# Kernel optimization log

Hardware: AMD Instinct MI355X
Metric: run time of the kernel (lower is better)

## Reference

```python
import jax, jax.numpy as jnp
import numpy as np

PAD_ID, BOS_ID, EOS_ID = 0, 2, 3
NHEAD = 8


def _sincos(T, d):
    pos = jnp.arange(T, dtype=jnp.float32)
    omega = jnp.exp(-jnp.arange(0, d, 2, dtype=jnp.float32) * (np.log(10000.0) / d))
    out = pos[:, None] * omega[None, :]  # [T, d/2]
    return jnp.stack([jnp.sin(out), jnp.cos(out)], axis=2).reshape(T, d)[None]  # [1,T,d]


def _ln(x, g, b, eps=1e-5):
    mu = x.mean(-1, keepdims=True)
    var = ((x - mu) ** 2).mean(-1, keepdims=True)
    return (x - mu) / jnp.sqrt(var + eps) * g + b


def _mha(q_in, kv_in, wqkv, bqkv, wo, bo, mask):
    B, Tq, d = q_in.shape
    Tk = kv_in.shape[1]
    hd = d // NHEAD
    q = q_in @ wqkv[:d].T + bqkv[:d]
    k = kv_in @ wqkv[d:2 * d].T + bqkv[d:2 * d]
    v = kv_in @ wqkv[2 * d:].T + bqkv[2 * d:]
    q = q.reshape(B, Tq, NHEAD, hd).transpose(0, 2, 1, 3)
    k = k.reshape(B, Tk, NHEAD, hd).transpose(0, 2, 1, 3)
    v = v.reshape(B, Tk, NHEAD, hd).transpose(0, 2, 1, 3)
    s = jnp.einsum('bhqd,bhkd->bhqk', q, k) / np.sqrt(hd)
    if mask is not None:
        s = s + mask
    a = jax.nn.softmax(s, axis=-1)
    o = jnp.einsum('bhqk,bhkd->bhqd', a, v).transpose(0, 2, 1, 3).reshape(B, Tq, d)
    return o @ wo.T + bo


def _last_logits(tokens, state, emb_table, qkv_w, qkv_b, out_w, out_b,
                 ffn_w1, ffn_b1, ffn_w2, ffn_b2, ln_g, ln_b):
    T = tokens.shape[1]
    d = emb_table.shape[1]
    x = emb_table[tokens] * np.sqrt(d) + _sincos(T, d)
    mask = jnp.where(jnp.tril(jnp.ones((T, T), bool)), 0.0, -jnp.inf)
    L = qkv_w.shape[0]
    for l in range(L):
        x = _ln(x + _mha(x, x, qkv_w[l, 0], qkv_b[l, 0], out_w[l, 0], out_b[l, 0], mask), ln_g[l, 0], ln_b[l, 0])
        x = _ln(x + _mha(x, state, qkv_w[l, 1], qkv_b[l, 1], out_w[l, 1], out_b[l, 1], None), ln_g[l, 1], ln_b[l, 1])
        h = jax.nn.gelu(x @ ffn_w1[l].T + ffn_b1[l], approximate=False)
        x = _ln(x + h @ ffn_w2[l].T + ffn_b2[l], ln_g[l, 2], ln_b[l, 2])
    return x[:, -1, :] @ emb_table.T  # tied output projection


def setup_inputs() -> dict:
    key = jax.random.key(0)
    ks = jax.random.split(key, 8)
    V, d, L, dff, B, K = 32000, 512, 4, 2048, 8, 64
    s = 0.02
    emb = jax.random.normal(ks[1], (V, d), jnp.float32) * s
    emb = emb.at[PAD_ID].set(0.0)  # padding_idx row is zero
    return {
        'state': jax.random.normal(ks[0], (B, K, d), jnp.float32),
        'emb_table': emb,
        'qkv_w': jax.random.normal(ks[2], (L, 2, 3 * d, d), jnp.float32) * s,
        'qkv_b': jnp.zeros((L, 2, 3 * d), jnp.float32),
        'out_w': jax.random.normal(ks[3], (L, 2, d, d), jnp.float32) * s,
        'out_b': jnp.zeros((L, 2, d), jnp.float32),
        'ffn_w1': jax.random.normal(ks[4], (L, dff, d), jnp.float32) * s,
        'ffn_b1': jnp.zeros((L, dff), jnp.float32),
        'ffn_w2': jax.random.normal(ks[5], (L, d, dff), jnp.float32) * s,
        'ffn_b2': jnp.zeros((L, d), jnp.float32),
        'ln_g': jnp.ones((L, 3, d), jnp.float32),
        'ln_b': jnp.zeros((L, 3, d), jnp.float32),
        'max_length': 16,
        'top_k': 50,
    }


def reference(state, emb_table, qkv_w, qkv_b, out_w, out_b, ffn_w1, ffn_b1,
              ffn_w2, ffn_b2, ln_g, ln_b, max_length, top_k):
    B = state.shape[0]
    generated = jnp.full((B, 1), BOS_ID, dtype=jnp.int32)
    finished = jnp.zeros(B, dtype=bool)
    key = jax.random.key(1)
    temperature = 1.0
    for t in range(max_length):
        # faithful naive recompute: full self+cross attention over generated prefix
        logits = _last_logits(generated, state, emb_table, qkv_w, qkv_b, out_w, out_b,
                              ffn_w1, ffn_b1, ffn_w2, ffn_b2, ln_g, ln_b)
        logits = logits / max(temperature, 1e-8)
        thr = jax.lax.top_k(logits, top_k)[0][:, -1:]
        filt = jnp.where(logits < thr, -jnp.inf, logits)
        nxt = jax.random.categorical(jax.random.fold_in(key, t), filt, axis=-1)
        nxt = jnp.where(finished, PAD_ID, nxt).astype(jnp.int32)
        generated = jnp.concatenate([generated, nxt[:, None]], axis=1)
        finished = finished | (nxt == EOS_ID)
    return generated
```

## Files before the change

kernel.cpp:

```cpp
#include <hip/hip_runtime.h>
#include <math.h>
#include <stdint.h>

#define D     512
#define DFF   2048
#define BB    8
#define NH    8
#define HD    64
#define NV    32000
#define NL    4
#define TMAX  17
#define KC    64
#define STEPS 16
#define KTOP  50
#define PAD_ID 0
#define BOS_ID 2
#define EOS_ID 3
#define SCOPE __HIP_MEMORY_SCOPE_AGENT

__device__ __forceinline__ float ld1(const float* p) {
  return __hip_atomic_load(p, __ATOMIC_RELAXED, SCOPE);
}
__device__ __forceinline__ void st1(float* p, float v) {
  __hip_atomic_store(p, v, __ATOMIC_RELAXED, SCOPE);
}
__device__ __forceinline__ float2 ld2(const float* p) {
  union { double d; float2 f; } u;
  u.d = __hip_atomic_load((const double*)p, __ATOMIC_RELAXED, SCOPE);
  return u.f;
}
__device__ __forceinline__ unsigned ldu(const unsigned* p) {
  return __hip_atomic_load(p, __ATOMIC_RELAXED, SCOPE);
}

__device__ __forceinline__ void tf2x32(unsigned k0, unsigned k1, unsigned x0, unsigned x1,
                                       unsigned& o0, unsigned& o1)
{
  unsigned ks2 = k0 ^ k1 ^ 0x1BD11BDAu;
#define TFR(r) { x0 += x1; x1 = (x1 << (r)) | (x1 >> (32 - (r))); x1 ^= x0; }
  x0 += k0; x1 += k1;
  TFR(13) TFR(15) TFR(26) TFR(6)
  x0 += k1;  x1 += ks2 + 1u;
  TFR(17) TFR(29) TFR(16) TFR(24)
  x0 += ks2; x1 += k0 + 2u;
  TFR(13) TFR(15) TFR(26) TFR(6)
  x0 += k0;  x1 += k1 + 3u;
  TFR(17) TFR(29) TFR(16) TFR(24)
  x0 += k1;  x1 += ks2 + 4u;
  TFR(13) TFR(15) TFR(26) TFR(6)
  o0 = x0 + ks2; o1 = x1 + k0 + 5u;
#undef TFR
}

__device__ __forceinline__ float wredf(float v) {
  for (int o = 32; o; o >>= 1) v += __shfl_xor(v, o, 64);
  return v;
}
__device__ __forceinline__ float wredmaxf(float v) {
  for (int o = 32; o; o >>= 1) v = fmaxf(v, __shfl_xor(v, o, 64));
  return v;
}
__device__ __forceinline__ unsigned monok(float f) {
  unsigned u = __float_as_uint(f);
  return (u & 0x80000000u) ? ~u : (u | 0x80000000u);
}

#define DOT8(a0,a1,x0,x1) (a0.x*x0.x + a0.y*x0.y + a0.z*x0.z + a0.w*x0.w + \
                           a1.x*x1.x + a1.y*x1.y + a1.z*x1.z + a1.w*x1.w)

__global__ void init_k(int* toks, unsigned* bars)
{
  int i = threadIdx.x;
  if (i < BB) toks[i * TMAX] = BOS_ID;
  for (int k = i; k < 2048; k += 256) bars[k] = 0u;
}

__global__ void cross_kv_k(const float* __restrict__ state, const float* __restrict__ qkvw,
                           const float* __restrict__ qkvb, float* __restrict__ cK,
                           float* __restrict__ cV)
{
  int gx = blockIdx.x, b = blockIdx.y, tid = threadIdx.x;
  int jblk = gx & 31, kpos = (gx >> 5) & 63, l = gx >> 11;
  int w = tid >> 6, lane = tid & 63;
  __shared__ __align__(16) float xsh[D];
  xsh[tid] = state[((size_t)b * KC + kpos) * D + tid];
  xsh[tid + 256] = state[((size_t)b * KC + kpos) * D + tid + 256];
  __syncthreads();
  for (int i = 0; i < 8; i++) {
    int j = jblk * 32 + w * 8 + i;
    int row = D + j;
    const float4* wr = (const float4*)(qkvw + (((size_t)l * 2 + 1) * (3 * D) + row) * D);
    const float4* x4 = (const float4*)xsh;
    float acc = 0.f;
    for (int e = lane; e < 128; e += 64) {
      float4 a = wr[e], xx = x4[e];
      acc += a.x * xx.x + a.y * xx.y + a.z * xx.z + a.w * xx.w;
    }
    acc = wredf(acc);
    if (lane == 0) {
      float v = acc + qkvb[((size_t)l * 2 + 1) * (3 * D) + row];
      float* dst = (j < D) ? cK : cV;
      int jj = (j < D) ? j : j - D;
      dst[(((size_t)l * BB + b) * KC + kpos) * D + jj] = v;
    }
  }
}

extern "C" __global__ void __launch_bounds__(512, 2)
decode_k(const float* __restrict__ emb, const float* __restrict__ qkv_w,
         const float* __restrict__ qkv_b, const float* __restrict__ out_w,
         const float* __restrict__ out_b, const float* __restrict__ f_w1,
         const float* __restrict__ f_b1, const float* __restrict__ f_w2,
         const float* __restrict__ f_b2, const float* __restrict__ lng,
         const float* __restrict__ lnb,
         const float* __restrict__ cK, const float* __restrict__ cV,
         float* Kc, float* Vc, float* qS, float* q2S,
         float* xt2, float* xt3, float* xt4, float* hB,
         float* xcur, float* lg, unsigned* bars, int* toks)
{
  const int tid = threadIdx.x, bid = blockIdx.x;
  const int g = bid & 7, gid = bid >> 3;
  const int w = tid >> 6, lane = tid & 63;
  unsigned gp = 0, glp = 0;
  int finished = 0;

  __shared__ __align__(16) unsigned char smem[65280];
  float* F = (float*)smem;
  float* sX1 = F;
  float* sX2 = F + 512;
  float* sQ  = F + 1024;
  float* sS  = F + 1536;
  float* sSP = F + 2080;
  float* sAO = F + 2624;
  float* sH  = F + 3136;
  float* sL  = F;
  float* sRed = F + 5184;
  unsigned short* key16 = (unsigned short*)smem;
  unsigned* histA = (unsigned*)(smem + 64000);
  unsigned* sKeys = (unsigned*)(smem + 64000);
  unsigned* sMeta = (unsigned*)(smem + 65024);
  float*    sWin  = (float*)(smem + 65056);
  int*      sWix  = (int*)(smem + 65088);

  const float SQD = (float)22.627416997969522;
  const float PEC = (float)(9.210340371976184 / 512.0);
  const float SQRT2 = (float)1.4142135623730951;

  auto gbarg = [&]() {
    asm volatile("s_waitcnt vmcnt(0)" ::: "memory");
    __syncthreads();
    ++gp;
    if (tid == 0) {
      unsigned* c = bars + g * 128;
      __hip_atomic_fetch_add(&c[(gid & 3) * 32], 1u, __ATOMIC_RELAXED, SCOPE);
      unsigned tgt = gp * 8u;
      for (;;) {
        unsigned s0 = ldu(&c[0]), s1 = ldu(&c[32]), s2 = ldu(&c[64]), s3 = ldu(&c[96]);
        unsigned mn = s0 < s1 ? s0 : s1;
        unsigned mn2 = s2 < s3 ? s2 : s3;
        if ((mn < mn2 ? mn : mn2) >= tgt) break;
        __builtin_amdgcn_s_sleep(1);
      }
    }
    asm volatile("" ::: "memory");
    __syncthreads();
  };
  auto gbarall = [&]() {
    asm volatile("s_waitcnt vmcnt(0)" ::: "memory");
    __syncthreads();
    ++glp;
    if (tid == 0) {
      unsigned* c = bars + 1024;
      __hip_atomic_fetch_add(&c[(bid & 15) * 32], 1u, __ATOMIC_RELAXED, SCOPE);
      unsigned tgt = glp * 16u;
      for (;;) {
        unsigned mn = 0xFFFFFFFFu;
#pragma unroll
        for (int i = 0; i < 16; i++) { unsigned x = ldu(&c[i * 32]); mn = x < mn ? x : mn; }
        if (mn >= tgt) break;
        __builtin_amdgcn_s_sleep(1);
      }
    }
    asm volatile("" ::: "memory");
    __syncthreads();
  };

  auto ln_local = [&](const float* src, const float* gamma, const float* beta, float* dst) {
    float v = ld1(src + tid);
    float s = wredf(v);
    if (lane == 0) sRed[w] = s;
    __syncthreads();
    float mu = (sRed[0] + sRed[1] + sRed[2] + sRed[3] +
                sRed[4] + sRed[5] + sRed[6] + sRed[7]) * (1.0f / 512.0f);
    __syncthreads();
    float d0 = v - mu;
    float q = wredf(d0 * d0);
    if (lane == 0) sRed[w] = q;
    __syncthreads();
    float sd = sqrtf((sRed[0] + sRed[1] + sRed[2] + sRed[3] +
                      sRed[4] + sRed[5] + sRed[6] + sRed[7]) * (1.0f / 512.0f) + 1e-5f);
    dst[tid] = d0 / sd * gamma[tid] + beta[tid];
    __syncthreads();
  };

  if (gid == 0) {
    float pe = (tid & 1) ? 1.0f : 0.0f;
    st1(&xcur[g * D + tid], emb[(size_t)BOS_ID * D + tid] * SQD + pe);
  }
  gbarg();

  for (int t = 0; t < STEPS; ++t) {
    const int T = t + 1;
    for (int l = 0; l < NL; ++l) {
      const float* wqkv0 = qkv_w + ((size_t)l * 2 + 0) * (3 * D) * D;
      const float* bqkv0 = qkv_b + ((size_t)l * 2 + 0) * (3 * D);
      const float* wqkv1 = qkv_w + ((size_t)l * 2 + 1) * (3 * D) * D;
      const float* bqkv1 = qkv_b + ((size_t)l * 2 + 1) * (3 * D);
      const float* wo0 = out_w + ((size_t)l * 2 + 0) * D * D;
      const float* bo0 = out_b + ((size_t)l * 2 + 0) * D;
      const float* wo1 = out_w + ((size_t)l * 2 + 1) * D * D;
      const float* bo1 = out_b + ((size_t)l * 2 + 1) * D;

      if (l == 0) {
        sX1[tid] = ld1(&xcur[g * D + tid]);
        __syncthreads();
      } else {
        ln_local(&xt4[g * D], lng + ((size_t)(l - 1) * 3 + 2) * D,
                 lnb + ((size_t)(l - 1) * 3 + 2) * D, sX1);
      }
      {
        const float4 x0 = ((const float4*)sX1)[lane], x1v = ((const float4*)sX1)[lane + 64];
        const int jbase = gid * 48 + w * 6;
        float4 wa[6], wb[6];
#pragma unroll
        for (int r = 0; r < 6; ++r) {
          const float4* w4 = (const float4*)(wqkv0 + (size_t)(jbase + r) * D);
          wa[r] = w4[lane]; wb[r] = w4[lane + 64];
        }
        float acc[6];
#pragma unroll
        for (int r = 0; r < 6; ++r) acc[r] = DOT8(wa[r], wb[r], x0, x1v);
#pragma unroll
        for (int o = 32; o; o >>= 1) {
#pragma unroll
          for (int r = 0; r < 6; ++r) acc[r] += __shfl_xor(acc[r], o, 64);
        }
        if (lane == 0) {
#pragma unroll
          for (int r = 0; r < 6; ++r) {
            int j = jbase + r;
            float v = acc[r] + bqkv0[j];
            if (j < D)          st1(&qS[g * D + j], v);
            else if (j < 2 * D) st1(&Kc[(((size_t)l * BB + g) * TMAX + t) * D + (j - D)], v);
            else                st1(&Vc[(((size_t)l * BB + g) * TMAX + t) * D + (j - 2 * D)], v);
          }
        }
      }
      gbarg();

      sQ[tid] = ld1(&qS[g * D + tid]);
      __syncthreads();
      if (tid < NH * T) {
        int h = tid / T, k = tid - h * T;
        const float4* Kr = (const float4*)(Kc + (((size_t)l * BB + g) * TMAX + k) * D + h * HD);
        const float4* q4 = (const float4*)(sQ + h * HD);
        float sc = 0.f;
#pragma unroll
        for (int e = 0; e < 16; ++e) {
          float4 a = Kr[e], b2 = q4[e];
          sc += a.x * b2.x + a.y * b2.y + a.z * b2.z + a.w * b2.w;
        }
        sS[h * TMAX + k] = sc * 0.125f;
      }
      __syncthreads();
      {
        int h = w;
        float v = (lane < T) ? sS[h * TMAX + lane] : -INFINITY;
        float m = wredmaxf(v);
        float p = (lane < T) ? expf(v - m) : 0.f;
        float den = wredf(p);
        if (lane < T) sSP[h * TMAX + lane] = p / den;
      }
      __syncthreads();
      {
        int h = w;
        const float* Vb = Vc + (((size_t)l * BB + g) * TMAX) * D + h * HD + lane;
        float acc = 0.f;
        for (int k = 0; k < T; ++k) acc += sSP[h * TMAX + k] * Vb[(size_t)k * D];
        sAO[tid] = acc;
      }
      __syncthreads();
      {
        const float4 x0 = ((const float4*)sAO)[lane], x1v = ((const float4*)sAO)[lane + 64];
        const int jbase = gid * 16 + w * 2;
        float4 wa[2], wb[2];
#pragma unroll
        for (int r = 0; r < 2; ++r) {
          const float4* w4 = (const float4*)(wo0 + (size_t)(jbase + r) * D);
          wa[r] = w4[lane]; wb[r] = w4[lane + 64];
        }
        float acc[2];
#pragma unroll
        for (int r = 0; r < 2; ++r) acc[r] = DOT8(wa[r], wb[r], x0, x1v);
#pragma unroll
        for (int o = 32; o; o >>= 1) {
#pragma unroll
          for (int r = 0; r < 2; ++r) acc[r] += __shfl_xor(acc[r], o, 64);
        }
        if (lane == 0) {
#pragma unroll
          for (int r = 0; r < 2; ++r) {
            int j = jbase + r;
            st1(&xt2[g * D + j], acc[r] + bo0[j] + sX1[j]);
          }
        }
      }
      gbarg();

      ln_local(&xt2[g * D], lng + ((size_t)l * 3 + 0) * D, lnb + ((size_t)l * 3 + 0) * D, sX2);
      {
        const float4 x0 = ((const float4*)sX2)[lane], x1v = ((const float4*)sX2)[lane + 64];
        const int jbase = gid * 16 + w * 2;
        float4 wa[2], wb[2];
#pragma unroll
        for (int r = 0; r < 2; ++r) {
          const float4* w4 = (const float4*)(wqkv1 + (size_t)(jbase + r) * D);
          wa[r] = w4[lane]; wb[r] = w4[lane + 64];
        }
        float acc[2];
#pragma unroll
        for (int r = 0; r < 2; ++r) acc[r] = DOT8(wa[r], wb[r], x0, x1v);
#pragma unroll
        for (int o = 32; o; o >>= 1) {
#pragma unroll
          for (int r = 0; r < 2; ++r) acc[r] += __shfl_xor(acc[r], o, 64);
        }
        if (lane == 0) {
#pragma unroll
          for (int r = 0; r < 2; ++r) {
            int j = jbase + r;
            st1(&q2S[g * D + j], acc[r] + bqkv1[j]);
          }
        }
      }
      gbarg();

      sQ[tid] = ld1(&q2S[g * D + tid]);
      __syncthreads();
      {
        int h = w, k = lane;
        const float4* Kr = (const float4*)(cK + (((size_t)l * BB + g) * KC + k) * D + h * HD);
        const float4* q4 = (const float4*)(sQ + h * HD);
        float sc = 0.f;
#pragma unroll
        for (int e = 0; e < 16; ++e) {
          float4 a = Kr[e], b2 = q4[e];
          sc += a.x * b2.x + a.y * b2.y + a.z * b2.z + a.w * b2.w;
        }
        sS[h * 64 + k] = sc * 0.125f;
      }
      __syncthreads();
      {
        int h = w;
        float v = sS[h * 64 + lane];
        float m = wredmaxf(v);
        float p = expf(v - m);
        float den = wredf(p);
        sSP[h * 64 + lane] = p / den;
      }
      __syncthreads();
      {
        int h = w;
        const float* Vb = cV + (((size_t)l * BB + g) * KC) * D + h * HD + lane;
        float acc = 0.f;
        for (int k = 0; k < KC; ++k) acc += sSP[h * 64 + k] * Vb[(size_t)k * D];
        sAO[tid] = acc;
      }
      __syncthreads();
      {
        const float4 x0 = ((const float4*)sAO)[lane], x1v = ((const float4*)sAO)[lane + 64];
        const int jbase = gid * 16 + w * 2;
        float4 wa[2], wb[2];
#pragma unroll
        for (int r = 0; r < 2; ++r) {
          const float4* w4 = (const float4*)(wo1 + (size_t)(jbase + r) * D);
          wa[r] = w4[lane]; wb[r] = w4[lane + 64];
        }
        float acc[2];
#pragma unroll
        for (int r = 0; r < 2; ++r) acc[r] = DOT8(wa[r], wb[r], x0, x1v);
#pragma unroll
        for (int o = 32; o; o >>= 1) {
#pragma unroll
          for (int r = 0; r < 2; ++r) acc[r] += __shfl_xor(acc[r], o, 64);
        }
        if (lane == 0) {
#pragma unroll
          for (int r = 0; r < 2; ++r) {
            int j = jbase + r;
            st1(&xt3[g * D + j], acc[r] + bo1[j] + sX2[j]);
          }
        }
      }
      gbarg();

      ln_local(&xt3[g * D], lng + ((size_t)l * 3 + 1) * D, lnb + ((size_t)l * 3 + 1) * D, sX1);
      {
        const float4 x0 = ((const float4*)sX1)[lane], x1v = ((const float4*)sX1)[lane + 64];
        const int jbase = gid * 64 + w * 8;
        float4 wa[8], wb[8];
#pragma unroll
        for (int r = 0; r < 8; ++r) {
          const float4* w4 = (const float4*)(f_w1 + (size_t)l * DFF * D + (size_t)(jbase + r) * D);
          wa[r] = w4[lane]; wb[r] = w4[lane + 64];
        }
        float acc[8];
#pragma unroll
        for (int r = 0; r < 8; ++r) acc[r] = DOT8(wa[r], wb[r], x0, x1v);
#pragma unroll
        for (int o = 32; o; o >>= 1) {
#pragma unroll
          for (int r = 0; r < 8; ++r) acc[r] += __shfl_xor(acc[r], o, 64);
        }
        if (lane == 0) {
#pragma unroll
          for (int r = 0; r < 8; ++r) {
            int j = jbase + r;
            float v = acc[r] + f_b1[(size_t)l * DFF + j];
            v = v * (erff(v / SQRT2) + 1.0f) / 2.0f;
            st1(&hB[g * DFF + j], v);
          }
        }
      }
      gbarg();

      for (int ii = tid; ii < 1024; ii += 512) {
        float2 v = ld2(&hB[g * DFF + 2 * ii]);
        sH[2 * ii] = v.x; sH[2 * ii + 1] = v.y;
      }
      __syncthreads();
      {
        float4 hx[8];
#pragma unroll
        for (int e = 0; e < 8; ++e) hx[e] = ((const float4*)sH)[lane + e * 64];
        const int jbase = gid * 16 + w * 2;
        float acc[2];
#pragma unroll
        for (int r = 0; r < 2; ++r) {
          const float4* w4 = (const float4*)(f_w2 + (size_t)l * D * DFF + (size_t)(jbase + r) * DFF);
          float a = 0.f;
#pragma unroll
          for (int e = 0; e < 8; ++e) {
            float4 aw = w4[lane + e * 64];
            a += aw.x * hx[e].x + aw.y * hx[e].y + aw.z * hx[e].z + aw.w * hx[e].w;
          }
          acc[r] = a;
        }
#pragma unroll
        for (int o = 32; o; o >>= 1) {
#pragma unroll
          for (int r = 0; r < 2; ++r) acc[r] += __shfl_xor(acc[r], o, 64);
        }
        if (lane == 0) {
#pragma unroll
          for (int r = 0; r < 2; ++r) {
            int j = jbase + r;
            st1(&xt4[g * D + j], acc[r] + f_b2[(size_t)l * D + j] + sX1[j]);
          }
        }
      }
      if (l < NL - 1) gbarg(); else gbarall();
    }

    for (int ii = tid; ii < 2048; ii += 512) {
      float2 v = ld2(&xt4[2 * ii]);
      sL[2 * ii] = v.x; sL[2 * ii + 1] = v.y;
    }
    __syncthreads();
    {
      int b = w;
      float vals[8]; float s = 0.f;
#pragma unroll
      for (int e = 0; e < 8; ++e) { vals[e] = sL[b * D + lane + e * 64]; s += vals[e]; }
      s = wredf(s);
      float mu = s * (1.0f / 512.0f);
      float q = 0.f;
#pragma unroll
      for (int e = 0; e < 8; ++e) { float d0 = vals[e] - mu; q += d0 * d0; }
      q = wredf(q);
      float sd = sqrtf(q * (1.0f / 512.0f) + 1e-5f);
      const float* ga = lng + 11 * D;
      const float* be = lnb + 11 * D;
#pragma unroll
      for (int e = 0; e < 8; ++e)
        sL[b * D + lane + e * 64] = (vals[e] - mu) / sd * ga[lane + e * 64] + be[lane + e * 64];
    }
    __syncthreads();
    for (int i = w; i < 125; i += 8) {
      int v = i * 256 + bid;
      const float4* er = (const float4*)(emb + (size_t)v * D);
      float4 e0 = er[lane], e1 = er[lane + 64];
      float acc[8];
#pragma unroll
      for (int b = 0; b < 8; b++) {
        const float4* x4 = (const float4*)(sL + b * D);
        float4 x0 = x4[lane], x1v = x4[lane + 64];
        acc[b] = DOT8(e0, e1, x0, x1v);
      }
#pragma unroll
      for (int o = 32; o; o >>= 1) {
#pragma unroll
        for (int b = 0; b < 8; b++) acc[b] += __shfl_xor(acc[b], o, 64);
      }
      if (lane == 0) {
#pragma unroll
        for (int b = 0; b < 8; b++) st1(&lg[(size_t)b * NV + v], acc[b]);
      }
    }
    gbarall();

    if (gid == 0) {
      int b = g;
      if (tid < 256) histA[tid] = 0u;
      __syncthreads();
      for (int v2 = tid; v2 < NV / 2; v2 += 512) {
        float2 f = ld2(&lg[(size_t)b * NV + 2 * v2]);
        unsigned u0 = monok(f.x), u1 = monok(f.y);
        key16[2 * v2] = (unsigned short)(u0 >> 16);
        key16[2 * v2 + 1] = (unsigned short)(u1 >> 16);
        atomicAdd(&histA[u0 >> 24], 1u);
        atomicAdd(&histA[u1 >> 24], 1u);
      }
      __syncthreads();
      if (tid == 0) {
        unsigned k = KTOP, cum = 0;
        for (int bin = 255; bin >= 0; bin--) {
          cum += histA[bin];
          if (cum >= k) { sMeta[0] = (unsigned)bin; sMeta[1] = k - (cum - histA[bin]); break; }
        }
      }
      __syncthreads();
      unsigned selHi = sMeta[0], rem1 = sMeta[1];
      if (tid < 256) histA[tid] = 0u;
      __syncthreads();
      for (int v = tid; v < NV; v += 512) {
        unsigned k16 = key16[v];
        if ((k16 >> 8) == selHi) atomicAdd(&histA[k16 & 255u], 1u);
      }
      __syncthreads();
      if (tid == 0) {
        unsigned k = rem1, cum = 0;
        for (int bin = 255; bin >= 0; bin--) {
          cum += histA[bin];
          if (cum >= k) { sMeta[2] = (selHi << 8) | (unsigned)bin; sMeta[1] = k - (cum - histA[bin]); break; }
        }
        sMeta[3] = 0u;
      }
      __syncthreads();
      unsigned P16 = sMeta[2], rem2 = sMeta[1];
      for (int v = tid; v < NV; v += 512) {
        if (key16[v] == (unsigned short)P16) {
          unsigned i = atomicAdd(&sMeta[3], 1u);
          if (i < 256) sKeys[i] = monok(ld1(&lg[(size_t)b * NV + v]));
        }
      }
      __syncthreads();
      if (tid == 0) {
        unsigned n = sMeta[3]; if (n > 256) n = 256;
        unsigned thr = 0;
        for (unsigned it = 0; it < rem2; ++it) {
          unsigned bestk = 0; int bj = 0;
          for (unsigned jx = 0; jx < n; jx++)
            if (sKeys[jx] > bestk) { bestk = sKeys[jx]; bj = (int)jx; }
          thr = bestk;
          sKeys[bj] = 0u;
        }
        sMeta[5] = (thr & 0x80000000u) ? (thr ^ 0x80000000u) : ~thr;
      }
      __syncthreads();
      float th = __uint_as_float(sMeta[5]);
      unsigned k0, k1;
      tf2x32(0u, 1u, 0u, (unsigned)t, k0, k1);
      float best = -INFINITY; int bi = NV;
      for (int v = tid; v < NV; v += 512) {
        if (key16[v] >= (unsigned short)P16) {
          float lo = ld1(&lg[(size_t)b * NV + v]);
          if (lo >= th) {
            unsigned o0, o1;
            tf2x32(k0, k1, 0u, (unsigned)(b * NV + v), o0, o1);
            unsigned bits = o0 ^ o1;
            unsigned ub = (bits >> 9) | 0x3f800000u;
            float fu = __uint_as_float(ub) - 1.0f;
            const float TINY = 1.17549435e-38f;
            float u = fu * (1.0f - TINY) + TINY;
            u = fmaxf(TINY, u);
            float gmb = -logf(-logf(u));
            float s = lo + gmb;
            if (s > best || (s == best && v < bi)) { best = s; bi = v; }
          }
        }
      }
      for (int o = 32; o; o >>= 1) {
        float ob = __shfl_xor(best, o, 64); int ox = __shfl_xor(bi, o, 64);
        if (ob > best || (ob == best && ox < bi)) { best = ob; bi = ox; }
      }
      if (lane == 0) { sWin[w] = best; sWix[w] = bi; }
      __syncthreads();
      if (tid == 0) {
        float bb = sWin[0]; int bx = sWix[0];
        for (int i2 = 1; i2 < 8; i2++) {
          if (sWin[i2] > bb || (sWin[i2] == bb && sWix[i2] < bx)) { bb = sWin[i2]; bx = sWix[i2]; }
        }
        int tok = bx;
        if (finished) tok = PAD_ID;
        toks[b * TMAX + t + 1] = tok;
        if (tok == EOS_ID) finished = 1;
        sMeta[4] = (unsigned)tok;
      }
      __syncthreads();
      {
        int tok = (int)sMeta[4];
        float omega = expf(-(float)(tid & ~1) * PEC);
        float val = (float)(t + 1) * omega;
        float pe = (tid & 1) ? cosf(val) : sinf(val);
        st1(&xcur[g * D + tid], emb[(size_t)tok * D + tid] * SQD + pe);
      }
    }
    gbarg();
  }
}

extern "C" void kernel_launch(void* const* d_in, const int* in_sizes, int n_in,
                              void* d_out, int out_size, void* d_ws, size_t ws_size,
                              hipStream_t stream)
{
  const float* state = (const float*)d_in[0];
  const float* emb   = (const float*)d_in[1];
  const float* qkv_w = (const float*)d_in[2];
  const float* qkv_b = (const float*)d_in[3];
  const float* out_w = (const float*)d_in[4];
  const float* out_b = (const float*)d_in[5];
  const float* f_w1  = (const float*)d_in[6];
  const float* f_b1  = (const float*)d_in[7];
  const float* f_w2  = (const float*)d_in[8];
  const float* f_b2  = (const float*)d_in[9];
  const float* lng   = (const float*)d_in[10];
  const float* lnb   = (const float*)d_in[11];

  float* ws = (float*)d_ws;
  float* cK   = ws;
  float* cV   = cK + (size_t)NL * BB * KC * D;
  float* Kc   = cV + (size_t)NL * BB * KC * D;
  float* Vc   = Kc + (size_t)NL * BB * TMAX * D;
  float* qS   = Vc + (size_t)NL * BB * TMAX * D;
  float* q2S  = qS + BB * D;
  float* xt2  = q2S + BB * D;
  float* xt3  = xt2 + BB * D;
  float* xt4  = xt3 + BB * D;
  float* hB   = xt4 + BB * D;
  float* xcur = hB + BB * DFF;
  float* lg   = xcur + BB * D;
  unsigned* bars = (unsigned*)(lg + (size_t)BB * NV);

  int* toks = (int*)d_out;

  init_k<<<1, 256, 0, stream>>>(toks, bars);
  cross_kv_k<<<dim3(NL * KC * 32, BB), 256, 0, stream>>>(state, qkv_w, qkv_b, cK, cV);
  decode_k<<<256, 512, 0, stream>>>(emb, qkv_w, qkv_b, out_w, out_b,
                                    f_w1, f_b1, f_w2, f_b2, lng, lnb,
                                    cK, cV, Kc, Vc, qS, q2S,
                                    xt2, xt3, xt4, hB, xcur, lg, bars, toks);
}
```

Before: 6.056 ms.

## Repartition decode kernel by (batch, head) to cut grid barriers per layer

```diff
diff --git a/kernel.cpp b/kernel.cpp
--- a/kernel.cpp
+++ b/kernel.cpp
@@ -114,33 +114,35 @@
          const float* __restrict__ f_b2, const float* __restrict__ lng,
          const float* __restrict__ lnb,
          const float* __restrict__ cK, const float* __restrict__ cV,
-         float* Kc, float* Vc, float* qS, float* q2S,
-         float* xt2, float* xt3, float* xt4, float* hB,
+         float* Kc, float* Vc, float* xt2p, float* xt3p, float* xt4p,
          float* xcur, float* lg, unsigned* bars, int* toks)
 {
   const int tid = threadIdx.x, bid = blockIdx.x;
-  const int g = bid & 7, gid = bid >> 3;
+  const int b = bid & 7, h = bid >> 3;
   const int w = tid >> 6, lane = tid & 63;
   unsigned gp = 0, glp = 0;
   int finished = 0;
 
   __shared__ __align__(16) unsigned char smem[65280];
   float* F = (float*)smem;
-  float* sX1 = F;
-  float* sX2 = F + 512;
-  float* sQ  = F + 1024;
-  float* sS  = F + 1536;
-  float* sSP = F + 2080;
-  float* sAO = F + 2624;
-  float* sH  = F + 3136;
-  float* sL  = F;
-  float* sRed = F + 5184;
+  float* sX1n = F;
+  float* sXn  = F + 512;
+  float* sQh  = F + 1024;
+  float* sKt  = F + 1088;
+  float* sVt  = F + 1152;
+  float* sS   = F + 1216;
+  float* sSP  = F + 1280;
+  float* sPart= F + 1344;
+  float* sAO  = F + 1856;
+  float* sH   = F + 1920;
+  float* sL   = F;
   unsigned short* key16 = (unsigned short*)smem;
   unsigned* histA = (unsigned*)(smem + 64000);
   unsigned* sKeys = (unsigned*)(smem + 64000);
   unsigned* sMeta = (unsigned*)(smem + 65024);
   float*    sWin  = (float*)(smem + 65056);
   int*      sWix  = (int*)(smem + 65088);
+  float*    sRed  = (float*)(smem + 65152);
 
   const float SQD = (float)22.627416997969522;
   const float PEC = (float)(9.210340371976184 / 512.0);
@@ -151,16 +153,10 @@
     __syncthreads();
     ++gp;
     if (tid == 0) {
-      unsigned* c = bars + g * 128;
-      __hip_atomic_fetch_add(&c[(gid & 3) * 32], 1u, __ATOMIC_RELAXED, SCOPE);
+      unsigned* c = bars + b * 32;
+      __hip_atomic_fetch_add(c, 1u, __ATOMIC_RELAXED, SCOPE);
       unsigned tgt = gp * 8u;
-      for (;;) {
-        unsigned s0 = ldu(&c[0]), s1 = ldu(&c[32]), s2 = ldu(&c[64]), s3 = ldu(&c[96]);
-        unsigned mn = s0 < s1 ? s0 : s1;
-        unsigned mn2 = s2 < s3 ? s2 : s3;
-        if ((mn < mn2 ? mn : mn2) >= tgt) break;
-        __builtin_amdgcn_s_sleep(1);
-      }
+      while (ldu(c) < tgt) __builtin_amdgcn_s_sleep(1);
     }
     asm volatile("" ::: "memory");
     __syncthreads();
@@ -170,42 +166,33 @@
     __syncthreads();
     ++glp;
     if (tid == 0) {
-      unsigned* c = bars + 1024;
-      __hip_atomic_fetch_add(&c[(bid & 15) * 32], 1u, __ATOMIC_RELAXED, SCOPE);
-      unsigned tgt = glp * 16u;
-      for (;;) {
-        unsigned mn = 0xFFFFFFFFu;
-#pragma unroll
-        for (int i = 0; i < 16; i++) { unsigned x = ldu(&c[i * 32]); mn = x < mn ? x : mn; }
-        if (mn >= tgt) break;
-        __builtin_amdgcn_s_sleep(1);
-      }
+      unsigned* c = bars + 512;
+      __hip_atomic_fetch_add(c, 1u, __ATOMIC_RELAXED, SCOPE);
+      unsigned tgt = glp * 64u;
+      while (ldu(c) < tgt) __builtin_amdgcn_s_sleep(1);
     }
     asm volatile("" ::: "memory");
     __syncthreads();
   };
 
-  auto ln_local = [&](const float* src, const float* gamma, const float* beta, float* dst) {
-    float v = ld1(src + tid);
-    float s = wredf(v);
+  auto lnvec = [&](float a, const float* ga, const float* be, float* dst) {
+    float s = wredf(a);
     if (lane == 0) sRed[w] = s;
     __syncthreads();
-    float mu = (sRed[0] + sRed[1] + sRed[2] + sRed[3] +
-                sRed[4] + sRed[5] + sRed[6] + sRed[7]) * (1.0f / 512.0f);
-    __syncthreads();
-    float d0 = v - mu;
+    float mu = (sRed[0]+sRed[1]+sRed[2]+sRed[3]+sRed[4]+sRed[5]+sRed[6]+sRed[7]) * (1.0f/512.0f);
+    __syncthreads();
+    float d0 = a - mu;
     float q = wredf(d0 * d0);
     if (lane == 0) sRed[w] = q;
     __syncthreads();
-    float sd = sqrtf((sRed[0] + sRed[1] + sRed[2] + sRed[3] +
-                      sRed[4] + sRed[5] + sRed[6] + sRed[7]) * (1.0f / 512.0f) + 1e-5f);
-    dst[tid] = d0 / sd * gamma[tid] + beta[tid];
+    float sd = sqrtf((sRed[0]+sRed[1]+sRed[2]+sRed[3]+sRed[4]+sRed[5]+sRed[6]+sRed[7]) * (1.0f/512.0f) + 1e-5f);
+    dst[tid] = d0 / sd * ga[tid] + be[tid];
     __syncthreads();
   };
 
-  if (gid == 0) {
+  if (bid < BB) {
     float pe = (tid & 1) ? 1.0f : 0.0f;
-    st1(&xcur[g * D + tid], emb[(size_t)BOS_ID * D + tid] * SQD + pe);
+    st1(&xcur[bid * D + tid], emb[(size_t)BOS_ID * D + tid] * SQD + pe);
   }
   gbarg();
 
@@ -220,307 +207,261 @@
       const float* bo0 = out_b + ((size_t)l * 2 + 0) * D;
       const float* wo1 = out_w + ((size_t)l * 2 + 1) * D * D;
       const float* bo1 = out_b + ((size_t)l * 2 + 1) * D;
+      const size_t kvbase = ((size_t)(b * NH + h) * NL + l) * TMAX * HD;
 
       if (l == 0) {
-        sX1[tid] = ld1(&xcur[g * D + tid]);
+        sX1n[tid] = ld1(&xcur[b * D + tid]);
         __syncthreads();
       } else {
-        ln_local(&xt4[g * D], lng + ((size_t)(l - 1) * 3 + 2) * D,
-                 lnb + ((size_t)(l - 1) * 3 + 2) * D, sX1);
-      }
-      {
-        const float4 x0 = ((const float4*)sX1)[lane], x1v = ((const float4*)sX1)[lane + 64];
-        const int jbase = gid * 48 + w * 6;
-        float4 wa[6], wb[6];
-#pragma unroll
-        for (int r = 0; r < 6; ++r) {
-          const float4* w4 = (const float4*)(wqkv0 + (size_t)(jbase + r) * D);
-          wa[r] = w4[lane]; wb[r] = w4[lane + 64];
-        }
-        float acc[6];
-#pragma unroll
-        for (int r = 0; r < 6; ++r) acc[r] = DOT8(wa[r], wb[r], x0, x1v);
-#pragma unroll
-        for (int o = 32; o; o >>= 1) {
-#pragma unroll
-          for (int r = 0; r < 6; ++r) acc[r] += __shfl_xor(acc[r], o, 64);
-        }
-        if (lane == 0) {
-#pragma unroll
-          for (int r = 0; r < 6; ++r) {
-            int j = jbase + r;
-            float v = acc[r] + bqkv0[j];
-            if (j < D)          st1(&qS[g * D + j], v);
-            else if (j < 2 * D) st1(&Kc[(((size_t)l * BB + g) * TMAX + t) * D + (j - D)], v);
-            else                st1(&Vc[(((size_t)l * BB + g) * TMAX + t) * D + (j - 2 * D)], v);
-          }
-        }
-      }
-      gbarg();
-
-      sQ[tid] = ld1(&qS[g * D + tid]);
-      __syncthreads();
-      if (tid < NH * T) {
-        int h = tid / T, k = tid - h * T;
-        const float4* Kr = (const float4*)(Kc + (((size_t)l * BB + g) * TMAX + k) * D + h * HD);
-        const float4* q4 = (const float4*)(sQ + h * HD);
-        float sc = 0.f;
-#pragma unroll
-        for (int e = 0; e < 16; ++e) {
-          float4 a = Kr[e], b2 = q4[e];
-          sc += a.x * b2.x + a.y * b2.y + a.z * b2.z + a.w * b2.w;
-        }
-        sS[h * TMAX + k] = sc * 0.125f;
-      }
-      __syncthreads();
-      {
-        int h = w;
-        float v = (lane < T) ? sS[h * TMAX + lane] : -INFINITY;
+        float a = 0.f;
+#pragma unroll
+        for (int s2 = 0; s2 < 8; ++s2) a += ld1(&xt4p[((size_t)b * 8 + s2) * D + tid]);
+        lnvec(a, lng + ((size_t)(l - 1) * 3 + 2) * D, lnb + ((size_t)(l - 1) * 3 + 2) * D, sX1n);
+      }
+      {
+        const float4* x4 = (const float4*)sX1n;
+        float4 x0 = x4[lane], x1v = x4[lane + 64];
+        for (int set = 0; set < 3; ++set) {
+          int rowbase = set * 512 + h * 64 + w * 8;
+          for (int pass = 0; pass < 2; ++pass) {
+            float4 wa[4], wb2[4];
+#pragma unroll
+            for (int r = 0; r < 4; ++r) {
+              const float4* w4 = (const float4*)(wqkv0 + (size_t)(rowbase + pass * 4 + r) * D);
+              wa[r] = w4[lane]; wb2[r] = w4[lane + 64];
+            }
+            float a4[4];
+#pragma unroll
+            for (int r = 0; r < 4; ++r) a4[r] = DOT8(wa[r], wb2[r], x0, x1v);
+#pragma unroll
+            for (int o = 32; o; o >>= 1) {
+#pragma unroll
+              for (int r = 0; r < 4; ++r) a4[r] += __shfl_xor(a4[r], o, 64);
+            }
+            if (lane == 0) {
+#pragma unroll
+              for (int r = 0; r < 4; ++r) {
+                int jj = w * 8 + pass * 4 + r;
+                int row = rowbase + pass * 4 + r;
+                float v = a4[r] + bqkv0[row];
+                if (set == 0)      sQh[jj] = v;
+                else if (set == 1) { st1(&Kc[kvbase + (size_t)t * HD + jj], v); sKt[jj] = v; }
+                else               { st1(&Vc[kvbase + (size_t)t * HD + jj], v); sVt[jj] = v; }
+              }
+            }
+          }
+        }
+      }
+      __syncthreads();
+      for (int k = w; k < T; k += 8) {
+        float kv = (k == t) ? sKt[lane] : Kc[kvbase + (size_t)k * HD + lane];
+        float sc = wredf(sQh[lane] * kv);
+        if (lane == 0) sS[k] = sc * 0.125f;
+      }
+      __syncthreads();
+      if (w == 0) {
+        float v = (lane < T) ? sS[lane] : -INFINITY;
         float m = wredmaxf(v);
         float p = (lane < T) ? expf(v - m) : 0.f;
         float den = wredf(p);
-        if (lane < T) sSP[h * TMAX + lane] = p / den;
-      }
-      __syncthreads();
-      {
-        int h = w;
-        const float* Vb = Vc + (((size_t)l * BB + g) * TMAX) * D + h * HD + lane;
+        if (lane < T) sSP[lane] = p / den;
+      }
+      __syncthreads();
+      {
         float acc = 0.f;
-        for (int k = 0; k < T; ++k) acc += sSP[h * TMAX + k] * Vb[(size_t)k * D];
-        sAO[tid] = acc;
-      }
-      __syncthreads();
-      {
-        const float4 x0 = ((const float4*)sAO)[lane], x1v = ((const float4*)sAO)[lane + 64];
-        const int jbase = gid * 16 + w * 2;
-        float4 wa[2], wb[2];
-#pragma unroll
-        for (int r = 0; r < 2; ++r) {
-          const float4* w4 = (const float4*)(wo0 + (size_t)(jbase + r) * D);
-          wa[r] = w4[lane]; wb[r] = w4[lane + 64];
-        }
-        float acc[2];
-#pragma unroll
-        for (int r = 0; r < 2; ++r) acc[r] = DOT8(wa[r], wb[r], x0, x1v);
-#pragma unroll
-        for (int o = 32; o; o >>= 1) {
-#pragma unroll
-          for (int r = 0; r < 2; ++r) acc[r] += __shfl_xor(acc[r], o, 64);
-        }
-        if (lane == 0) {
-#pragma unroll
-          for (int r = 0; r < 2; ++r) {
-            int j = jbase + r;
-            st1(&xt2[g * D + j], acc[r] + bo0[j] + sX1[j]);
-          }
-        }
+        for (int k = w; k < T; k += 8) {
+          float vv = (k == t) ? sVt[lane] : Vc[kvbase + (size_t)k * HD + lane];
+          acc += sSP[k] * vv;
+        }
+        sPart[w * 64 + lane] = acc;
+      }
+      __syncthreads();
+      if (tid < 64) {
+        float a = 0.f;
+#pragma unroll
+        for (int i = 0; i < 8; ++i) a += sPart[i * 64 + tid];
+        sAO[tid] = a;
+      }
+      __syncthreads();
+      {
+        int j = tid;
+        const float4* wr4 = (const float4*)(wo0 + (size_t)j * D + h * HD);
+        float acc = 0.f;
+#pragma unroll
+        for (int e = 0; e < 16; ++e) {
+          float4 aw = wr4[e];
+          acc += aw.x * sAO[e*4] + aw.y * sAO[e*4+1] + aw.z * sAO[e*4+2] + aw.w * sAO[e*4+3];
+        }
+        if (h == 0) acc += bo0[j] + sX1n[j];
+        st1(&xt2p[((size_t)b * 8 + h) * D + j], acc);
       }
       gbarg();
 
-      ln_local(&xt2[g * D], lng + ((size_t)l * 3 + 0) * D, lnb + ((size_t)l * 3 + 0) * D, sX2);
-      {
-        const float4 x0 = ((const float4*)sX2)[lane], x1v = ((const float4*)sX2)[lane + 64];
-        const int jbase = gid * 16 + w * 2;
-        float4 wa[2], wb[2];
-#pragma unroll
-        for (int r = 0; r < 2; ++r) {
-          const float4* w4 = (const float4*)(wqkv1 + (size_t)(jbase + r) * D);
-          wa[r] = w4[lane]; wb[r] = w4[lane + 64];
-        }
-        float acc[2];
-#pragma unroll
-        for (int r = 0; r < 2; ++r) acc[r] = DOT8(wa[r], wb[r], x0, x1v);
-#pragma unroll
-        for (int o = 32; o; o >>= 1) {
-#pragma unroll
-          for (int r = 0; r < 2; ++r) acc[r] += __shfl_xor(acc[r], o, 64);
-        }
-        if (lane == 0) {
-#pragma unroll
-          for (int r = 0; r < 2; ++r) {
-            int j = jbase + r;
-            st1(&q2S[g * D + j], acc[r] + bqkv1[j]);
-          }
-        }
+      {
+        float a = 0.f;
+#pragma unroll
+        for (int s2 = 0; s2 < 8; ++s2) a += ld1(&xt2p[((size_t)b * 8 + s2) * D + tid]);
+        lnvec(a, lng + ((size_t)l * 3 + 0) * D, lnb + ((size_t)l * 3 + 0) * D, sXn);
+      }
+      {
+        const float4* x4 = (const float4*)sXn;
+        float4 x0 = x4[lane], x1v = x4[lane + 64];
+        for (int pass = 0; pass < 2; ++pass) {
+          float4 wa[4], wb2[4];
+#pragma unroll
+          for (int r = 0; r < 4; ++r) {
+            const float4* w4 = (const float4*)(wqkv1 + (size_t)(h * 64 + w * 8 + pass * 4 + r) * D);
+            wa[r] = w4[lane]; wb2[r] = w4[lane + 64];
+          }
+          float a4[4];
+#pragma unroll
+          for (int r = 0; r < 4; ++r) a4[r] = DOT8(wa[r], wb2[r], x0, x1v);
+#pragma unroll
+          for (int o = 32; o; o >>= 1) {
+#pragma unroll
+            for (int r = 0; r < 4; ++r) a4[r] += __shfl_xor(a4[r], o, 64);
+          }
+          if (lane == 0) {
+#pragma unroll
+            for (int r = 0; r < 4; ++r) {
+              int jj = w * 8 + pass * 4 + r;
+              sQh[jj] = a4[r] + bqkv1[h * 64 + jj];
+            }
+          }
+        }
+      }
+      __syncthreads();
+      {
+        size_t cbase = (((size_t)l * BB + b) * KC) * D + h * HD;
+        for (int k = w; k < KC; k += 8) {
+          float sc = wredf(sQh[lane] * cK[cbase + (size_t)k * D + lane]);
+          if (lane == 0) sS[k] = sc * 0.125f;
+        }
+        __syncthreads();
+        if (w == 0) {
+          float v = sS[lane];
+          float m = wredmaxf(v);
+          float p = expf(v - m);
+          float den = wredf(p);
+          sSP[lane] = p / den;
+        }
+        __syncthreads();
+        float acc = 0.f;
+        for (int k = w; k < KC; k += 8) acc += sSP[k] * cV[cbase + (size_t)k * D + lane];
+        sPart[w * 64 + lane] = acc;
+      }
+      __syncthreads();
+      if (tid < 64) {
+        float a = 0.f;
+#pragma unroll
+        for (int i = 0; i < 8; ++i) a += sPart[i * 64 + tid];
+        sAO[tid] = a;
+      }
+      __syncthreads();
+      {
+        int j = tid;
+        const float4* wr4 = (const float4*)(wo1 + (size_t)j * D + h * HD);
+        float acc = 0.f;
+#pragma unroll
+        for (int e = 0; e < 16; ++e) {
+          float4 aw = wr4[e];
+          acc += aw.x * sAO[e*4] + aw.y * sAO[e*4+1] + aw.z * sAO[e*4+2] + aw.w * sAO[e*4+3];
+        }
+        if (h == 0) acc += bo1[j] + sXn[j];
+        st1(&xt3p[((size_t)b * 8 + h) * D + j], acc);
       }
       gbarg();
 
-      sQ[tid] = ld1(&q2S[g * D + tid]);
-      __syncthreads();
-      {
-        int h = w, k = lane;
-        const float4* Kr = (const float4*)(cK + (((size_t)l * BB + g) * KC + k) * D + h * HD);
-        const float4* q4 = (const float4*)(sQ + h * HD);
-        float sc = 0.f;
-#pragma unroll
-        for (int e = 0; e < 16; ++e) {
-          float4 a = Kr[e], b2 = q4[e];
-          sc += a.x * b2.x + a.y * b2.y + a.z * b2.z + a.w * b2.w;
-        }
-        sS[h * 64 + k] = sc * 0.125f;
-      }
-      __syncthreads();
-      {
-        int h = w;
-        float v = sS[h * 64 + lane];
-        float m = wredmaxf(v);
-        float p = expf(v - m);
-        float den = wredf(p);
-        sSP[h * 64 + lane] = p / den;
-      }
-      __syncthreads();
-      {
-        int h = w;
-        const float* Vb = cV + (((size_t)l * BB + g) * KC) * D + h * HD + lane;
+      {
+        float a = 0.f;
+#pragma unroll
+        for (int s2 = 0; s2 < 8; ++s2) a += ld1(&xt3p[((size_t)b * 8 + s2) * D + tid]);
+        lnvec(a, lng + ((size_t)l * 3 + 1) * D, lnb + ((size_t)l * 3 + 1) * D, sXn);
+      }
+      {
+        const float4* x4 = (const float4*)sXn;
+        float4 x0 = x4[lane], x1v = x4[lane + 64];
+        for (int pass = 0; pass < 8; ++pass) {
+          int rl0 = w * 32 + pass * 4;
+          float4 wa[4], wb2[4];
+#pragma unroll
+          for (int r = 0; r < 4; ++r) {
+            const float4* w4 = (const float4*)(f_w1 + (size_t)l * DFF * D + (size_t)(h * 256 + rl0 + r) * D);
+            wa[r] = w4[lane]; wb2[r] = w4[lane + 64];
+          }
+          float a4[4];
+#pragma unroll
+          for (int r = 0; r < 4; ++r) a4[r] = DOT8(wa[r], wb2[r], x0, x1v);
+#pragma unroll
+          for (int o = 32; o; o >>= 1) {
+#pragma unroll
+            for (int r = 0; r < 4; ++r) a4[r] += __shfl_xor(a4[r], o, 64);
+          }
+          if (lane == 0) {
+#pragma unroll
+            for (int r = 0; r < 4; ++r) {
+              float v = a4[r] + f_b1[(size_t)l * DFF + h * 256 + rl0 + r];
+              v = v * (erff(v / SQRT2) + 1.0f) / 2.0f;
+              sH[rl0 + r] = v;
+            }
+          }
+        }
+      }
+      __syncthreads();
+      {
+        int j = tid;
+        const float4* wr4 = (const float4*)(f_w2 + (size_t)l * D * DFF + (size_t)j * DFF + h * 256);
         float acc = 0.f;
-        for (int k = 0; k < KC; ++k) acc += sSP[h * 64 + k] * Vb[(size_t)k * D];
-        sAO[tid] = acc;
-      }
-      __syncthreads();
-      {
-        const float4 x0 = ((const float4*)sAO)[lane], x1v = ((const float4*)sAO)[lane + 64];
-        const int jbase = gid * 16 + w * 2;
-        float4 wa[2], wb[2];
-#pragma unroll
-        for (int r = 0; r < 2; ++r) {
-          const float4* w4 = (const float4*)(wo1 + (size_t)(jbase + r) * D);
-          wa[r] = w4[lane]; wb[r] = w4[lane + 64];
-        }
-        float acc[2];
-#pragma unroll
-        for (int r = 0; r < 2; ++r) acc[r] = DOT8(wa[r], wb[r], x0, x1v);
-#pragma unroll
-        for (int o = 32; o; o >>= 1) {
-#pragma unroll
-          for (int r = 0; r < 2; ++r) acc[r] += __shfl_xor(acc[r], o, 64);
-        }
-        if (lane == 0) {
-#pragma unroll
-          for (int r = 0; r < 2; ++r) {
-            int j = jbase + r;
-            st1(&xt3[g * D + j], acc[r] + bo1[j] + sX2[j]);
-          }
-        }
-      }
-      gbarg();
-
-      ln_local(&xt3[g * D], lng + ((size_t)l * 3 + 1) * D, lnb + ((size_t)l * 3 + 1) * D, sX1);
-      {
-        const float4 x0 = ((const float4*)sX1)[lane], x1v = ((const float4*)sX1)[lane + 64];
-        const int jbase = gid * 64 + w * 8;
-        float4 wa[8], wb[8];
-#pragma unroll
-        for (int r = 0; r < 8; ++r) {
-          const float4* w4 = (const float4*)(f_w1 + (size_t)l * DFF * D + (size_t)(jbase + r) * D);
-          wa[r] = w4[lane]; wb[r] = w4[lane + 64];
-        }
-        float acc[8];
-#pragma unroll
-        for (int r = 0; r < 8; ++r) acc[r] = DOT8(wa[r], wb[r], x0, x1v);
-#pragma unroll
-        for (int o = 32; o; o >>= 1) {
-#pragma unroll
-          for (int r = 0; r < 8; ++r) acc[r] += __shfl_xor(acc[r], o, 64);
-        }
-        if (lane == 0) {
-#pragma unroll
-          for (int r = 0; r < 8; ++r) {
-            int j = jbase + r;
-            float v = acc[r] + f_b1[(size_t)l * DFF + j];
-            v = v * (erff(v / SQRT2) + 1.0f) / 2.0f;
-            st1(&hB[g * DFF + j], v);
-          }
-        }
-      }
-      gbarg();
-
-      for (int ii = tid; ii < 1024; ii += 512) {
-        float2 v = ld2(&hB[g * DFF + 2 * ii]);
-        sH[2 * ii] = v.x; sH[2 * ii + 1] = v.y;
-      }
-      __syncthreads();
-      {
-        float4 hx[8];
-#pragma unroll
-        for (int e = 0; e < 8; ++e) hx[e] = ((const float4*)sH)[lane + e * 64];
-        const int jbase = gid * 16 + w * 2;
-        float acc[2];
-#pragma unroll
-        for (int r = 0; r < 2; ++r) {
-          const float4* w4 = (const float4*)(f_w2 + (size_t)l * D * DFF + (size_t)(jbase + r) * DFF);
-          float a = 0.f;
-#pragma unroll
-          for (int e = 0; e < 8; ++e) {
-            float4 aw = w4[lane + e * 64];
-            a += aw.x * hx[e].x + aw.y * hx[e].y + aw.z * hx[e].z + aw.w * hx[e].w;
-          }
-          acc[r] = a;
-        }
-#pragma unroll
-        for (int o = 32; o; o >>= 1) {
-#pragma unroll
-          for (int r = 0; r < 2; ++r) acc[r] += __shfl_xor(acc[r], o, 64);
-        }
-        if (lane == 0) {
-#pragma unroll
-          for (int r = 0; r < 2; ++r) {
-            int j = jbase + r;
-            st1(&xt4[g * D + j], acc[r] + f_b2[(size_t)l * D + j] + sX1[j]);
-          }
-        }
+#pragma unroll 8
+        for (int e = 0; e < 64; ++e) {
+          float4 aw = wr4[e];
+          acc += aw.x * sH[e*4] + aw.y * sH[e*4+1] + aw.z * sH[e*4+2] + aw.w * sH[e*4+3];
+        }
+        if (h == 0) acc += f_b2[(size_t)l * D + j] + sXn[j];
+        st1(&xt4p[((size_t)b * 8 + h) * D + j], acc);
       }
       if (l < NL - 1) gbarg(); else gbarall();
     }
 
-    for (int ii = tid; ii < 2048; ii += 512) {
-      float2 v = ld2(&xt4[2 * ii]);
-      sL[2 * ii] = v.x; sL[2 * ii + 1] = v.y;
-    }
-    __syncthreads();
     {
-      int b = w;
-      float vals[8]; float s = 0.f;
-#pragma unroll
-      for (int e = 0; e < 8; ++e) { vals[e] = sL[b * D + lane + e * 64]; s += vals[e]; }
-      s = wredf(s);
-      float mu = s * (1.0f / 512.0f);
-      float q = 0.f;
-#pragma unroll
-      for (int e = 0; e < 8; ++e) { float d0 = vals[e] - mu; q += d0 * d0; }
-      q = wredf(q);
-      float sd = sqrtf(q * (1.0f / 512.0f) + 1e-5f);
+      float accb[8];
+#pragma unroll
+      for (int bb = 0; bb < 8; ++bb) {
+        float a = 0.f;
+#pragma unroll
+        for (int s2 = 0; s2 < 8; ++s2) a += ld1(&xt4p[((size_t)bb * 8 + s2) * D + tid]);
+        accb[bb] = a;
+      }
       const float* ga = lng + 11 * D;
       const float* be = lnb + 11 * D;
 #pragma unroll
-      for (int e = 0; e < 8; ++e)
-        sL[b * D + lane + e * 64] = (vals[e] - mu) / sd * ga[lane + e * 64] + be[lane + e * 64];
-    }
-    __syncthreads();
-    for (int i = w; i < 125; i += 8) {
-      int v = i * 256 + bid;
+      for (int bb = 0; bb < 8; ++bb)
+        lnvec(accb[bb], ga, be, sL + bb * 512);
+    }
+    for (int i = w; i < 500; i += 8) {
+      int v = i * 64 + bid;
       const float4* er = (const float4*)(emb + (size_t)v * D);
       float4 e0 = er[lane], e1 = er[lane + 64];
       float acc[8];
 #pragma unroll
-      for (int b = 0; b < 8; b++) {
-        const float4* x4 = (const float4*)(sL + b * D);
+      for (int bb = 0; bb < 8; bb++) {
+        const float4* x4 = (const float4*)(sL + bb * 512);
         float4 x0 = x4[lane], x1v = x4[lane + 64];
-        acc[b] = DOT8(e0, e1, x0, x1v);
+        acc[bb] = DOT8(e0, e1, x0, x1v);
       }
 #pragma unroll
       for (int o = 32; o; o >>= 1) {
 #pragma unroll
-        for (int b = 0; b < 8; b++) acc[b] += __shfl_xor(acc[b], o, 64);
+        for (int bb = 0; bb < 8; bb++) acc[bb] += __shfl_xor(acc[bb], o, 64);
       }
       if (lane == 0) {
 #pragma unroll
-        for (int b = 0; b < 8; b++) st1(&lg[(size_t)b * NV + v], acc[b]);
+        for (int bb = 0; bb < 8; bb++) st1(&lg[(size_t)bb * NV + v], acc[bb]);
       }
     }
     gbarall();
 
-    if (gid == 0) {
-      int b = g;
+    if (bid < BB) {
       if (tid < 256) histA[tid] = 0u;
       __syncthreads();
       for (int v2 = tid; v2 < NV / 2; v2 += 512) {
@@ -607,9 +548,9 @@
       if (lane == 0) { sWin[w] = best; sWix[w] = bi; }
       __syncthreads();
       if (tid == 0) {
-        float bb = sWin[0]; int bx = sWix[0];
+        float bb2 = sWin[0]; int bx = sWix[0];
         for (int i2 = 1; i2 < 8; i2++) {
-          if (sWin[i2] > bb || (sWin[i2] == bb && sWix[i2] < bx)) { bb = sWin[i2]; bx = sWix[i2]; }
+          if (sWin[i2] > bb2 || (sWin[i2] == bb2 && sWix[i2] < bx)) { bb2 = sWin[i2]; bx = sWix[i2]; }
         }
         int tok = bx;
         if (finished) tok = PAD_ID;
@@ -623,7 +564,7 @@
         float omega = expf(-(float)(tid & ~1) * PEC);
         float val = (float)(t + 1) * omega;
         float pe = (tid & 1) ? cosf(val) : sinf(val);
-        st1(&xcur[g * D + tid], emb[(size_t)tok * D + tid] * SQD + pe);
+        st1(&xcur[b * D + tid], emb[(size_t)tok * D + tid] * SQD + pe);
       }
     }
     gbarg();
@@ -651,14 +592,11 @@
   float* cK   = ws;
   float* cV   = cK + (size_t)NL * BB * KC * D;
   float* Kc   = cV + (size_t)NL * BB * KC * D;
-  float* Vc   = Kc + (size_t)NL * BB * TMAX * D;
-  float* qS   = Vc + (size_t)NL * BB * TMAX * D;
-  float* q2S  = qS + BB * D;
-  float* xt2  = q2S + BB * D;
-  float* xt3  = xt2 + BB * D;
-  float* xt4  = xt3 + BB * D;
-  float* hB   = xt4 + BB * D;
-  float* xcur = hB + BB * DFF;
+  float* Vc   = Kc + (size_t)BB * NH * NL * TMAX * HD;
+  float* xt2p = Vc + (size_t)BB * NH * NL * TMAX * HD;
+  float* xt3p = xt2p + (size_t)BB * 8 * D;
+  float* xt4p = xt3p + (size_t)BB * 8 * D;
+  float* xcur = xt4p + (size_t)BB * 8 * D;
   float* lg   = xcur + BB * D;
   unsigned* bars = (unsigned*)(lg + (size_t)BB * NV);
 
@@ -666,8 +604,8 @@
 
   init_k<<<1, 256, 0, stream>>>(toks, bars);
   cross_kv_k<<<dim3(NL * KC * 32, BB), 256, 0, stream>>>(state, qkv_w, qkv_b, cK, cV);
-  decode_k<<<256, 512, 0, stream>>>(emb, qkv_w, qkv_b, out_w, out_b,
-                                    f_w1, f_b1, f_w2, f_b2, lng, lnb,
-                                    cK, cV, Kc, Vc, qS, q2S,
-                                    xt2, xt3, xt4, hB, xcur, lg, bars, toks);
-}
+  decode_k<<<64, 512, 0, stream>>>(emb, qkv_w, qkv_b, out_w, out_b,
+                                   f_w1, f_b1, f_w2, f_b2, lng, lnb,
+                                   cK, cV, Kc, Vc, xt2p, xt3p, xt4p,
+                                   xcur, lg, bars, toks);
+}
```

Result: slower. 7.816 ms (+29.1%).
